# Kernel optimization log

Hardware: AMD Instinct MI355X
Metric: run time of the kernel (lower is better)

The kernel has to match this reference:

```python
import math
import jax, jax.numpy as jnp
import numpy as np

HID, NHEADS, MEM, LIM = 1024, 16, 512, 2048
HEAD = HID // NHEADS  # 64


def _skew(X, pad_value):
    # shift row m right by m steps: [B, M, L] -> [B, M, M+L]
    B, M, L = X.shape
    X = jnp.pad(X, ((0, 0), (0, 0), (0, M + 1)), constant_values=pad_value)
    X = X.reshape(B, -1)[:, :-M]
    return X.reshape(B, M, M + L)


def _unskew(X):
    # reverse of _skew: [B, M, M+L] -> [B, M, L]
    B, M, LM = X.shape
    L = LM - M
    X = jnp.pad(X.reshape(B, -1), ((0, 0), (0, M)))
    return X.reshape(B, M, LM + 1)[:, :, :L]


def _heads(x):
    # [B, S, K*D] -> [B*K, S, D]
    B, S, _ = x.shape
    return x.reshape(B, S, NHEADS, HEAD).transpose(0, 2, 1, 3).reshape(B * NHEADS, S, HEAD)


def setup_inputs() -> dict:
    key = jax.random.key(0)
    ks = jax.random.split(key, 8)
    B = 8
    s = 1.0 / math.sqrt(HID)
    return {
        "query": jax.random.normal(ks[0], (B, MEM, HID), jnp.float32),
        "key": jax.random.normal(ks[1], (B, MEM + LIM, HID), jnp.float32),
        "value": jax.random.normal(ks[2], (B, MEM + LIM, HID), jnp.float32),
        "key_pe": jax.random.normal(ks[3], (1, HEAD, LIM), jnp.float32),
        "Wq": jax.random.normal(ks[4], (HID, HID), jnp.float32) * s,
        "Wk": jax.random.normal(ks[5], (HID, HID), jnp.float32) * s,
        "Wv": jax.random.normal(ks[6], (HID, HID), jnp.float32) * s,
        "Wo": jax.random.normal(ks[7], (HID, HID), jnp.float32) * s,
    }


def reference(query, key, value, key_pe, Wq, Wk, Wv, Wo):
    B = query.shape[0]
    q = _heads(query @ Wq.T)   # [B*K, M, D]
    k = _heads(key @ Wk.T)     # [B*K, M+L, D]
    v = _heads(value @ Wv.T)   # [B*K, M+L, D]
    # content term via skew/unskew trick
    attn_cont = _unskew(jnp.einsum('bmd,bnd->bmn', q, k))  # [B*K, M, L]
    # relative-position term
    attn_pos = jnp.einsum('bmd,dl->bml', q, key_pe[0])     # [B*K, M, L]
    attn = jax.nn.softmax((attn_cont + attn_pos) / math.sqrt(HEAD), axis=-1)
    out = jnp.matmul(_skew(attn, 0.0), v)                  # [B*K, M, D]
    out = out.reshape(B, NHEADS, MEM, HEAD).transpose(0, 2, 1, 3).reshape(B, MEM, HID)
    return out @ Wo.T
```

## Files before the change

### kernel.cpp

```cpp
#include <hip/hip_runtime.h>
#include <hip/hip_bf16.h>
#include <stdint.h>


typedef __attribute__((ext_vector_type(8))) __bf16 bfrag;
typedef __attribute__((ext_vector_type(4))) float f4;

#define DEVFN static __device__ __forceinline__

DEVFN void glds16(const void* g, void* l) {
  __builtin_amdgcn_global_load_lds((const __attribute__((address_space(1))) void*)g,
                                   (__attribute__((address_space(3))) void*)l, 16, 0, 0);
}

DEVFN bfrag cvt8(const float* p) {
  f4 a = *(const f4*)p;
  f4 b = *(const f4*)(p + 4);
  bfrag v;
  v[0] = (__bf16)a.x; v[1] = (__bf16)a.y; v[2] = (__bf16)a.z; v[3] = (__bf16)a.w;
  v[4] = (__bf16)b.x; v[5] = (__bf16)b.y; v[6] = (__bf16)b.z; v[7] = (__bf16)b.w;
  return v;
}

__global__ __launch_bounds__(256) void conv4(const float* __restrict__ a0, const float* __restrict__ a1,
                                             const float* __restrict__ a2, const float* __restrict__ a3,
                                             __bf16* __restrict__ d0, __bf16* __restrict__ d1,
                                             __bf16* __restrict__ d2, __bf16* __restrict__ d3) {
  int bx = blockIdx.x;
  int sel = bx >> 9;
  const float* s = sel == 0 ? a0 : sel == 1 ? a1 : sel == 2 ? a2 : a3;
  __bf16* d = sel == 0 ? d0 : sel == 1 ? d1 : sel == 2 ? d2 : d3;
  int i = ((bx & 511) * 256 + (int)threadIdx.x) * 8;
  *(bfrag*)(d + i) = cvt8(s + i);
}

__global__ __launch_bounds__(256) void convin(const float* __restrict__ q, const float* __restrict__ k,
                                              const float* __restrict__ v,
                                              __bf16* __restrict__ qd, __bf16* __restrict__ kd,
                                              __bf16* __restrict__ vd) {
  int bx = blockIdx.x;
  const float* s; __bf16* d; int lb;
  if (bx < 2048)       { s = q; d = qd; lb = bx; }
  else if (bx < 12288) { s = k; d = kd; lb = bx - 2048; }
  else                 { s = v; d = vd; lb = bx - 12288; }
  int i = (lb * 256 + (int)threadIdx.x) * 8;
  *(bfrag*)(d + i) = cvt8(s + i);
}

__global__ __launch_bounds__(256) void pek(const float* __restrict__ pe,
                                           __bf16* __restrict__ peT) {
  int i = blockIdx.x * 256 + threadIdx.x;
  if (i < 64 * 2048) {
    int d = i >> 11, l = i & 2047;
    peT[(size_t)(l + 64) * 64 + d] = (__bf16)pe[i];
  } else {
    int zi = i - 64 * 2048;
    int row = zi >> 6, dd = zi & 63;
    int r = row < 64 ? row : (2112 + row - 64);
    peT[(size_t)r * 64 + dd] = (__bf16)0.f;
  }
}

DEVFN void stageA_row(const float* ap, __bf16* lds, int arow, int ahalf) {
  const f4* p = (const f4*)ap;
#pragma unroll
  for (int q = 0; q < 4; ++q) {
    f4 a = p[2 * q], b = p[2 * q + 1];
    bfrag v;
    v[0] = (__bf16)a.x; v[1] = (__bf16)a.y; v[2] = (__bf16)a.z; v[3] = (__bf16)a.w;
    v[4] = (__bf16)b.x; v[5] = (__bf16)b.y; v[6] = (__bf16)b.z; v[7] = (__bf16)b.w;
    int ch = (4 * ahalf + q) ^ (arow & 7);
    *(bfrag*)&lds[arow * 64 + ch * 8] = v;
  }
}

template <int AMODE, typename AT>
__global__ __launch_bounds__(256) void projk(const AT* __restrict__ Aq, const AT* __restrict__ Ak,
                                             const AT* __restrict__ Av,
                                             const __bf16* __restrict__ Wqb, const __bf16* __restrict__ Wkb,
                                             const __bf16* __restrict__ Wvb,
                                             __bf16* __restrict__ qws, __bf16* __restrict__ kws,
                                             __bf16* __restrict__ vtws) {
  __shared__ alignas(16) __bf16 Alds[128 * 64];
  __shared__ alignas(16) __bf16 Blds[128 * 64];
  int bx = blockIdx.x;
  const AT* A; const __bf16* B; __bf16* C; int nb, lb, rpb, trans;
  if (bx < 256)       { A = Aq; B = Wqb; C = qws;  lb = bx;        nb = 256;  rpb = 4;  trans = 0; }
  else if (bx < 1536) { A = Ak; B = Wkb; C = kws;  lb = bx - 256;  nb = 1280; rpb = 20; trans = 0; }
  else                { A = Av; B = Wvb; C = vtws; lb = bx - 1536; nb = 1280; rpb = 20; trans = 1; }

  const int tid = threadIdx.x;
  const int lane = tid & 63, wv = tid >> 6;
  const int wr = wv >> 1, wc = wv & 1;
  const int g = lane >> 4, cl = lane & 15;

  int v = (lb & 7) * (nb >> 3) + (lb >> 3);
  const int trow = v >> 3;
  const int r0 = trow * 128, c0 = (v & 7) * 128;

  f4 acc[4][4] = {};

  for (int k0 = 0; k0 < 1024; k0 += 64) {
    __syncthreads();
#pragma unroll
    for (int i = 0; i < 4; ++i) {
      int slot = tid + 256 * i;
      int row = slot >> 3, ch = slot & 7;
      glds16(B + (size_t)(c0 + row) * 1024 + k0 + ((ch ^ (row & 7)) << 3),
             &Blds[slot << 3]);
      if constexpr (AMODE == 1)
        glds16(A + (size_t)(r0 + row) * 1024 + k0 + ((ch ^ (row & 7)) << 3),
               &Alds[slot << 3]);
    }
    if constexpr (AMODE == 0)
      stageA_row(A + (size_t)(r0 + (tid >> 1)) * 1024 + k0 + (tid & 1) * 32,
                 Alds, tid >> 1, tid & 1);
    __syncthreads();
#pragma unroll
    for (int kc = 0; kc < 2; ++kc) {
      bfrag af[4], bfv[4];
#pragma unroll
      for (int i = 0; i < 4; ++i) {
        int rA = 64 * wr + 16 * i + cl;
        af[i] = *(const bfrag*)&Alds[rA * 64 + (((g + 4 * kc) ^ (rA & 7)) << 3)];
        int rB = 64 * wc + 16 * i + cl;
        bfv[i] = *(const bfrag*)&Blds[rB * 64 + (((g + 4 * kc) ^ (rB & 7)) << 3)];
      }
#pragma unroll
      for (int am = 0; am < 4; ++am)
#pragma unroll
        for (int bn = 0; bn < 4; ++bn)
          acc[am][bn] =
              __builtin_amdgcn_mfma_f32_16x16x32_bf16(af[am], bfv[bn], acc[am][bn], 0, 0, 0);
    }
  }

  int Sseq = rpb << 7;
  int b = trow / rpb;
  int sbase = r0 - b * Sseq;
#pragma unroll
  for (int am = 0; am < 4; ++am)
#pragma unroll
    for (int bn = 0; bn < 4; ++bn) {
      int jg = c0 + 64 * wc + 16 * bn + cl;
      int h = jg >> 6, d = jg & 63;
#pragma unroll
      for (int r = 0; r < 4; ++r) {
        int s = sbase + 64 * wr + 16 * am + 4 * g + r;
        size_t dst = trans ? ((size_t)(b * 16 + h) * 64 + d) * 2560 + s
                           : ((size_t)(b * 16 + h) * Sseq + s) * 64 + d;
        C[dst] = (__bf16)acc[am][bn][r];
      }
    }
}

__global__ __launch_bounds__(256) void gemm_out(const __bf16* __restrict__ A,
                                                const __bf16* __restrict__ B,
                                                float* __restrict__ C) {
  __shared__ alignas(16) __bf16 Alds[128 * 64];
  __shared__ alignas(16) __bf16 Blds[128 * 64];
  const int tid = threadIdx.x;
  const int lane = tid & 63, wv = tid >> 6;
  const int wr = wv >> 1, wc = wv & 1;
  const int g = lane >> 4, cl = lane & 15;

  int bx = blockIdx.x;
  int v = (bx & 7) * 32 + (bx >> 3);
  const int r0 = (v >> 3) * 128, c0 = (v & 7) * 128;

  f4 acc[4][4] = {};
  for (int k0 = 0; k0 < 1024; k0 += 64) {
    __syncthreads();
#pragma unroll
    for (int i = 0; i < 4; ++i) {
      int slot = tid + 256 * i;
      int row = slot >> 3, ch = slot & 7;
      glds16(B + (size_t)(c0 + row) * 1024 + k0 + ((ch ^ (row & 7)) << 3),
             &Blds[slot << 3]);
      glds16(A + (size_t)(r0 + row) * 1024 + k0 + ((ch ^ (row & 7)) << 3),
             &Alds[slot << 3]);
    }
    __syncthreads();
#pragma unroll
    for (int kc = 0; kc < 2; ++kc) {
      bfrag af[4], bfv[4];
#pragma unroll
      for (int i = 0; i < 4; ++i) {
        int rA = 64 * wr + 16 * i + cl;
        af[i] = *(const bfrag*)&Alds[rA * 64 + (((g + 4 * kc) ^ (rA & 7)) << 3)];
        int rB = 64 * wc + 16 * i + cl;
        bfv[i] = *(const bfrag*)&Blds[rB * 64 + (((g + 4 * kc) ^ (rB & 7)) << 3)];
      }
#pragma unroll
      for (int am = 0; am < 4; ++am)
#pragma unroll
        for (int bn = 0; bn < 4; ++bn)
          acc[am][bn] =
              __builtin_amdgcn_mfma_f32_16x16x32_bf16(af[am], bfv[bn], acc[am][bn], 0, 0, 0);
    }
  }
#pragma unroll
  for (int am = 0; am < 4; ++am)
#pragma unroll
    for (int bn = 0; bn < 4; ++bn)
#pragma unroll
      for (int r = 0; r < 4; ++r) {
        int rg = r0 + 64 * wr + 16 * am + 4 * g + r;
        int jg = c0 + 64 * wc + 16 * bn + cl;
        C[(size_t)rg * 1024 + jg] = acc[am][bn][r];
      }
}

#define SCL 0.18033688011112042f
#define FMX 20.0f

__global__ __launch_bounds__(256) void attnk(const __bf16* __restrict__ qws,
                                             const __bf16* __restrict__ kws,
                                             const __bf16* __restrict__ vtws,
                                             const __bf16* __restrict__ pews,
                                             __bf16* __restrict__ obuf) {
  __shared__ alignas(16) __bf16 Ks[64 * 64];
  __shared__ alignas(16) __bf16 QVs[64 * 64];
  __shared__ alignas(16) __bf16 PPs[64 * 64];
  __shared__ alignas(16) __bf16 Pbs[64 * 128];

  int bx = blockIdx.x;
  int vv = (bx & 7) * 128 + (bx >> 3);
  int bh = vv >> 3, mt = vv & 7;
  int m0 = mt * 64;
  const __bf16* qb = qws + (size_t)bh * 512 * 64;
  const __bf16* kb = kws + (size_t)bh * 2560 * 64;
  const __bf16* vb = vtws + (size_t)bh * 64 * 2560;

  const int tid = threadIdx.x;
  const int lane = tid & 63, w = tid >> 6;
  const int g = lane >> 4, cl = lane & 15;

#pragma unroll
  for (int i = 0; i < 2; ++i) {
    int slot = tid + 256 * i;
    int row = slot >> 3, ch = slot & 7;
    glds16(qb + (size_t)(m0 + row) * 64 + ((ch ^ (row & 7)) << 3), &QVs[slot << 3]);
  }
  __syncthreads();
  bfrag qf_all[4][2];
#pragma unroll
  for (int rb = 0; rb < 4; ++rb) {
    int rq = 16 * rb + cl;
#pragma unroll
    for (int kc = 0; kc < 2; ++kc)
      qf_all[rb][kc] = *(const bfrag*)&QVs[rq * 64 + (((g + 4 * kc) ^ (rq & 7)) << 3)];
  }

  f4 o[4] = {};
  float lsum[4] = {};

  for (int t = 0; t < 33; ++t) {
    int n0 = m0 + 64 * t;
    __syncthreads();
#pragma unroll
    for (int i = 0; i < 2; ++i) {
      int slot = tid + 256 * i;
      int row = slot >> 3, ch = slot & 7;
      glds16(kb + (size_t)(n0 + row) * 64 + ((ch ^ (row & 7)) << 3), &Ks[slot << 3]);
      glds16(vb + (size_t)row * 2560 + n0 + ((ch ^ (row & 7)) << 3), &QVs[slot << 3]);
      glds16(pews + (size_t)(64 * (t + 1) + row) * 64 + ((ch ^ (row & 7)) << 3),
             &PPs[slot << 3]);
    }
    __syncthreads();

    f4 sc[4] = {};
    __builtin_amdgcn_s_setprio(1);
#pragma unroll
    for (int kc = 0; kc < 2; ++kc)
#pragma unroll
      for (int cb = 0; cb < 4; ++cb) {
        int rk = 16 * cb + cl;
        bfrag kf = *(const bfrag*)&Ks[rk * 64 + (((g + 4 * kc) ^ (rk & 7)) << 3)];
        sc[cb] = __builtin_amdgcn_mfma_f32_16x16x32_bf16(qf_all[w][kc], kf, sc[cb], 0, 0, 0);
      }
    f4 pbacc[4] = {};
#pragma unroll
    for (int kc = 0; kc < 2; ++kc) {
      int rp = 16 * w + cl;
      bfrag pf = *(const bfrag*)&PPs[rp * 64 + (((g + 4 * kc) ^ (rp & 7)) << 3)];
#pragma unroll
      for (int rb = 0; rb < 4; ++rb)
        pbacc[rb] = __builtin_amdgcn_mfma_f32_16x16x32_bf16(qf_all[rb][kc], pf, pbacc[rb], 0, 0, 0);
    }
    __builtin_amdgcn_s_setprio(0);
    {
      int half = (t & 1) << 6;
      int c2 = 16 * w + cl;
#pragma unroll
      for (int rb = 0; rb < 4; ++rb)
#pragma unroll
        for (int r = 0; r < 4; ++r)
          Pbs[(16 * rb + 4 * g + r) * 128 + half + c2] = (__bf16)pbacc[rb][r];
    }
    __syncthreads();

    bool edge = (t == 0) || (t == 32);
#pragma unroll
    for (int r = 0; r < 4; ++r) {
      int jm = 16 * w + 4 * g + r;
#pragma unroll
      for (int cb = 0; cb < 4; ++cb) {
        int jn = 16 * cb + cl;
        int l = 64 * t + jn - jm;
        float pv = (float)Pbs[jm * 128 + (l & 127)];
        float ex = fmaf(sc[cb][r] + pv, SCL, -FMX);
        if (edge) ex = ((unsigned)l < 2048u) ? ex : -1e30f;
        float p = __builtin_amdgcn_exp2f(ex);
        lsum[r] += p;
        PPs[jm * 64 + (((jn >> 3) ^ (jm & 7)) << 3) + (jn & 7)] = (__bf16)p;
      }
    }

    __builtin_amdgcn_s_setprio(1);
#pragma unroll
    for (int kc = 0; kc < 2; ++kc) {
      int rp2 = 16 * w + cl;
      bfrag pa = *(const bfrag*)&PPs[rp2 * 64 + (((g + 4 * kc) ^ (rp2 & 7)) << 3)];
#pragma unroll
      for (int cb = 0; cb < 4; ++cb) {
        int rv = 16 * cb + cl;
        bfrag vf = *(const bfrag*)&QVs[rv * 64 + (((g + 4 * kc) ^ (rv & 7)) << 3)];
        o[cb] = __builtin_amdgcn_mfma_f32_16x16x32_bf16(pa, vf, o[cb], 0, 0, 0);
      }
    }
    __builtin_amdgcn_s_setprio(0);
  }

#pragma unroll
  for (int r = 0; r < 4; ++r)
#pragma unroll
    for (int off = 1; off < 16; off <<= 1) lsum[r] += __shfl_xor(lsum[r], off);

  int b = bh >> 4, h = bh & 15;
#pragma unroll
  for (int cb = 0; cb < 4; ++cb)
#pragma unroll
    for (int r = 0; r < 4; ++r) {
      int m = m0 + 16 * w + 4 * g + r;
      int d = 16 * cb + cl;
      obuf[((size_t)(b * 512 + m)) * 1024 + h * 64 + d] = (__bf16)(o[cb][r] / lsum[r]);
    }
}

extern "C" void kernel_launch(void* const* d_in, const int* in_sizes, int n_in,
                              void* d_out, int out_size, void* d_ws, size_t ws_size,
                              hipStream_t stream) {
  const float* query = (const float*)d_in[0];
  const float* key   = (const float*)d_in[1];
  const float* value = (const float*)d_in[2];
  const float* keype = (const float*)d_in[3];
  const float* Wq    = (const float*)d_in[4];
  const float* Wk    = (const float*)d_in[5];
  const float* Wv    = (const float*)d_in[6];
  const float* Wo    = (const float*)d_in[7];
  float* out = (float*)d_out;
  (void)in_sizes; (void)n_in; (void)out_size;

  char* ws = (char*)d_ws;
  size_t off = 0;
  auto alloc = [&](size_t bytes) {
    void* p = ws + off;
    off += (bytes + 255) & ~(size_t)255;
    return p;
  };
  __bf16* Wqb  = (__bf16*)alloc((size_t)1024 * 1024 * 2);
  __bf16* Wkb  = (__bf16*)alloc((size_t)1024 * 1024 * 2);
  __bf16* Wvb  = (__bf16*)alloc((size_t)1024 * 1024 * 2);
  __bf16* Wob  = (__bf16*)alloc((size_t)1024 * 1024 * 2);
  __bf16* peT  = (__bf16*)alloc((size_t)2176 * 64 * 2);
  __bf16* qws  = (__bf16*)alloc((size_t)128 * 512 * 64 * 2);
  __bf16* kws  = (__bf16*)alloc((size_t)128 * 2560 * 64 * 2);
  __bf16* vtws = (__bf16*)alloc((size_t)128 * 2560 * 64 * 2);

  const size_t NEED = (size_t)194 * 1024 * 1024;
  bool big = ws_size >= NEED;

  conv4<<<2048, 256, 0, stream>>>(Wq, Wk, Wv, Wo, Wqb, Wkb, Wvb, Wob);
  pek<<<544, 256, 0, stream>>>(keype, peT);

  __bf16* obuf;
  if (big) {
    __bf16* qbf = (__bf16*)alloc((size_t)8 * 512 * 1024 * 2);
    __bf16* kbf = (__bf16*)alloc((size_t)8 * 2560 * 1024 * 2);
    __bf16* vbf = (__bf16*)alloc((size_t)8 * 2560 * 1024 * 2);
    obuf = qbf;
    convin<<<22528, 256, 0, stream>>>(query, key, value, qbf, kbf, vbf);
    projk<1, __bf16><<<2816, 256, 0, stream>>>(qbf, kbf, vbf, Wqb, Wkb, Wvb,
                                               qws, kws, vtws);
  } else {
    obuf = (__bf16*)alloc((size_t)4096 * 1024 * 2);
    projk<0, float><<<2816, 256, 0, stream>>>(query, key, value, Wqb, Wkb, Wvb,
                                              qws, kws, vtws);
  }

  attnk<<<1024, 256, 0, stream>>>(qws, kws, vtws, peT, obuf);
  gemm_out<<<256, 256, 0, stream>>>(obuf, Wob, out);
}
```

Measured before the change: 395.0 us.

## Replace bf16 projection GEMM with 256x256-tile double-buffered 8-wave kernel

```diff
diff --git a/kernel.cpp b/kernel.cpp
--- a/kernel.cpp
+++ b/kernel.cpp
@@ -61,6 +61,156 @@
   }
 }
 
+DEVFN bfrag rdfrag(const __bf16* L, int row, int kc, int g) {
+  return *(const bfrag*)&L[row * 64 + (((g + 4 * kc) ^ (row & 7)) << 3)];
+}
+
+__global__ __launch_bounds__(512, 2) void projk8(const __bf16* __restrict__ qbf,
+                                                 const __bf16* __restrict__ kbf,
+                                                 const __bf16* __restrict__ vbf,
+                                                 const __bf16* __restrict__ Wqb,
+                                                 const __bf16* __restrict__ Wkb,
+                                                 const __bf16* __restrict__ Wvb,
+                                                 __bf16* __restrict__ qws,
+                                                 __bf16* __restrict__ kws,
+                                                 __bf16* __restrict__ vtws) {
+  __shared__ alignas(16) __bf16 AL[2][256 * 64];
+  __shared__ alignas(16) __bf16 BL[2][256 * 64];
+
+  int bx = blockIdx.x;
+  int v = (bx & 7) * 88 + (bx >> 3);
+  int rt = v >> 2, ct = v & 3;
+
+  const __bf16* A; const __bf16* W; __bf16* C; int lrt, S, trans;
+  if (rt < 16)      { A = qbf; W = Wqb; C = qws;  lrt = rt;      S = 512;  trans = 0; }
+  else if (rt < 96) { A = kbf; W = Wkb; C = kws;  lrt = rt - 16; S = 2560; trans = 0; }
+  else              { A = vbf; W = Wvb; C = vtws; lrt = rt - 96; S = 2560; trans = 1; }
+  const int r0 = lrt * 256, c0 = ct * 256;
+  const size_t aoff = (size_t)r0 * 1024, boff = (size_t)c0 * 1024;
+
+  const int tid = threadIdx.x;
+  const int lane = tid & 63, wv = tid >> 6;
+  const int wr = wv >> 2, wc = wv & 3;
+  const int g = lane >> 4, cl = lane & 15;
+
+  auto stage_half = [&](int s, int k0, int h) {
+#pragma unroll
+    for (int j = 0; j < 2; ++j) {
+      int slot = h * 1024 + j * 512 + tid;
+      int row = slot >> 3, ch = slot & 7;
+      size_t gof = (size_t)row * 1024 + k0 + ((ch ^ (row & 7)) << 3);
+      glds16(A + aoff + gof, &AL[s][slot << 3]);
+      glds16(W + boff + gof, &BL[s][slot << 3]);
+    }
+  };
+
+  f4 acc[8][4] = {};
+
+  stage_half(0, 0, 0);
+  stage_half(0, 0, 1);
+  asm volatile("s_waitcnt vmcnt(0)" ::: "memory");
+  __builtin_amdgcn_s_barrier();
+
+  for (int kt = 0; kt < 16; ++kt) {
+    const int s = kt & 1;
+    const __bf16* As = AL[s];
+    const __bf16* Bs = BL[s];
+    const int k0n = (kt + 1) * 64;
+    bfrag af[8], b01[4], b23[4];
+
+#pragma unroll
+    for (int mf = 0; mf < 4; ++mf)
+#pragma unroll
+      for (int kc = 0; kc < 2; ++kc)
+        af[mf * 2 + kc] = rdfrag(As, wr * 128 + mf * 16 + cl, kc, g);
+#pragma unroll
+    for (int nf = 0; nf < 2; ++nf)
+#pragma unroll
+      for (int kc = 0; kc < 2; ++kc)
+        b01[nf * 2 + kc] = rdfrag(Bs, wc * 64 + nf * 16 + cl, kc, g);
+    if (kt < 15) stage_half(s ^ 1, k0n, 0);
+    __builtin_amdgcn_s_barrier();
+    __builtin_amdgcn_s_setprio(1);
+#pragma unroll
+    for (int mf = 0; mf < 4; ++mf)
+#pragma unroll
+      for (int nf = 0; nf < 2; ++nf)
+#pragma unroll
+        for (int kc = 0; kc < 2; ++kc)
+          acc[mf][nf] = __builtin_amdgcn_mfma_f32_16x16x32_bf16(
+              af[mf * 2 + kc], b01[nf * 2 + kc], acc[mf][nf], 0, 0, 0);
+    __builtin_amdgcn_s_setprio(0);
+    __builtin_amdgcn_s_barrier();
+
+#pragma unroll
+    for (int nf = 0; nf < 2; ++nf)
+#pragma unroll
+      for (int kc = 0; kc < 2; ++kc)
+        b23[nf * 2 + kc] = rdfrag(Bs, wc * 64 + (2 + nf) * 16 + cl, kc, g);
+    if (kt < 15) stage_half(s ^ 1, k0n, 1);
+    __builtin_amdgcn_s_barrier();
+    __builtin_amdgcn_s_setprio(1);
+#pragma unroll
+    for (int mf = 0; mf < 4; ++mf)
+#pragma unroll
+      for (int nf = 0; nf < 2; ++nf)
+#pragma unroll
+        for (int kc = 0; kc < 2; ++kc)
+          acc[mf][2 + nf] = __builtin_amdgcn_mfma_f32_16x16x32_bf16(
+              af[mf * 2 + kc], b23[nf * 2 + kc], acc[mf][2 + nf], 0, 0, 0);
+    __builtin_amdgcn_s_setprio(0);
+    __builtin_amdgcn_s_barrier();
+
+#pragma unroll
+    for (int mf = 0; mf < 4; ++mf)
+#pragma unroll
+      for (int kc = 0; kc < 2; ++kc)
+        af[mf * 2 + kc] = rdfrag(As, wr * 128 + (4 + mf) * 16 + cl, kc, g);
+    __builtin_amdgcn_s_barrier();
+    __builtin_amdgcn_s_setprio(1);
+#pragma unroll
+    for (int mf = 0; mf < 4; ++mf)
+#pragma unroll
+      for (int nf = 0; nf < 2; ++nf)
+#pragma unroll
+        for (int kc = 0; kc < 2; ++kc)
+          acc[4 + mf][nf] = __builtin_amdgcn_mfma_f32_16x16x32_bf16(
+              af[mf * 2 + kc], b01[nf * 2 + kc], acc[4 + mf][nf], 0, 0, 0);
+    __builtin_amdgcn_s_setprio(0);
+    __builtin_amdgcn_s_barrier();
+
+    __builtin_amdgcn_s_setprio(1);
+#pragma unroll
+    for (int mf = 0; mf < 4; ++mf)
+#pragma unroll
+      for (int nf = 0; nf < 2; ++nf)
+#pragma unroll
+        for (int kc = 0; kc < 2; ++kc)
+          acc[4 + mf][2 + nf] = __builtin_amdgcn_mfma_f32_16x16x32_bf16(
+              af[mf * 2 + kc], b23[nf * 2 + kc], acc[4 + mf][2 + nf], 0, 0, 0);
+    __builtin_amdgcn_s_setprio(0);
+    if (kt < 15) asm volatile("s_waitcnt vmcnt(0)" ::: "memory");
+    __builtin_amdgcn_s_barrier();
+  }
+
+  int b = r0 / S;
+  int sbase = r0 - b * S;
+#pragma unroll
+  for (int mf = 0; mf < 8; ++mf)
+#pragma unroll
+    for (int nf = 0; nf < 4; ++nf) {
+      int jg = c0 + wc * 64 + nf * 16 + cl;
+      int h = jg >> 6, d = jg & 63;
+#pragma unroll
+      for (int r = 0; r < 4; ++r) {
+        int srow = sbase + wr * 128 + mf * 16 + 4 * g + r;
+        size_t dst = trans ? ((size_t)(b * 16 + h) * 64 + d) * 2560 + srow
+                           : ((size_t)(b * 16 + h) * S + srow) * 64 + d;
+        C[dst] = (__bf16)acc[mf][nf][r];
+      }
+    }
+}
+
 DEVFN void stageA_row(const float* ap, __bf16* lds, int arow, int ahalf) {
   const f4* p = (const f4*)ap;
 #pragma unroll
@@ -74,17 +224,16 @@
   }
 }
 
-template <int AMODE, typename AT>
-__global__ __launch_bounds__(256) void projk(const AT* __restrict__ Aq, const AT* __restrict__ Ak,
-                                             const AT* __restrict__ Av,
-                                             const __bf16* __restrict__ Wqb, const __bf16* __restrict__ Wkb,
-                                             const __bf16* __restrict__ Wvb,
-                                             __bf16* __restrict__ qws, __bf16* __restrict__ kws,
-                                             __bf16* __restrict__ vtws) {
+__global__ __launch_bounds__(256) void projk_f32(const float* __restrict__ Aq, const float* __restrict__ Ak,
+                                                 const float* __restrict__ Av,
+                                                 const __bf16* __restrict__ Wqb, const __bf16* __restrict__ Wkb,
+                                                 const __bf16* __restrict__ Wvb,
+                                                 __bf16* __restrict__ qws, __bf16* __restrict__ kws,
+                                                 __bf16* __restrict__ vtws) {
   __shared__ alignas(16) __bf16 Alds[128 * 64];
   __shared__ alignas(16) __bf16 Blds[128 * 64];
   int bx = blockIdx.x;
-  const AT* A; const __bf16* B; __bf16* C; int nb, lb, rpb, trans;
+  const float* A; const __bf16* B; __bf16* C; int nb, lb, rpb, trans;
   if (bx < 256)       { A = Aq; B = Wqb; C = qws;  lb = bx;        nb = 256;  rpb = 4;  trans = 0; }
   else if (bx < 1536) { A = Ak; B = Wkb; C = kws;  lb = bx - 256;  nb = 1280; rpb = 20; trans = 0; }
   else                { A = Av; B = Wvb; C = vtws; lb = bx - 1536; nb = 1280; rpb = 20; trans = 1; }
@@ -108,13 +257,9 @@
       int row = slot >> 3, ch = slot & 7;
       glds16(B + (size_t)(c0 + row) * 1024 + k0 + ((ch ^ (row & 7)) << 3),
              &Blds[slot << 3]);
-      if constexpr (AMODE == 1)
-        glds16(A + (size_t)(r0 + row) * 1024 + k0 + ((ch ^ (row & 7)) << 3),
-               &Alds[slot << 3]);
-    }
-    if constexpr (AMODE == 0)
-      stageA_row(A + (size_t)(r0 + (tid >> 1)) * 1024 + k0 + (tid & 1) * 32,
-                 Alds, tid >> 1, tid & 1);
+    }
+    stageA_row(A + (size_t)(r0 + (tid >> 1)) * 1024 + k0 + (tid & 1) * 32,
+               Alds, tid >> 1, tid & 1);
     __syncthreads();
 #pragma unroll
     for (int kc = 0; kc < 2; ++kc) {
@@ -391,12 +536,11 @@
     __bf16* vbf = (__bf16*)alloc((size_t)8 * 2560 * 1024 * 2);
     obuf = qbf;
     convin<<<22528, 256, 0, stream>>>(query, key, value, qbf, kbf, vbf);
-    projk<1, __bf16><<<2816, 256, 0, stream>>>(qbf, kbf, vbf, Wqb, Wkb, Wvb,
-                                               qws, kws, vtws);
+    projk8<<<704, 512, 0, stream>>>(qbf, kbf, vbf, Wqb, Wkb, Wvb, qws, kws, vtws);
   } else {
     obuf = (__bf16*)alloc((size_t)4096 * 1024 * 2);
-    projk<0, float><<<2816, 256, 0, stream>>>(query, key, value, Wqb, Wkb, Wvb,
-                                              qws, kws, vtws);
+    projk_f32<<<2816, 256, 0, stream>>>(query, key, value, Wqb, Wkb, Wvb,
+                                        qws, kws, vtws);
   }
 
   attnk<<<1024, 256, 0, stream>>>(qws, kws, vtws, peT, obuf);
```

Result: slower. 407.6 us (+3.2%).

## Double-buffer A tile in projection and output GEMMs with prefetch and MFMA priority

Applied to the files above, without the earlier changes.

```diff
diff --git a/kernel.cpp b/kernel.cpp
--- a/kernel.cpp
+++ b/kernel.cpp
@@ -61,6 +61,111 @@
   }
 }
 
+DEVFN bfrag rdfrag(const __bf16* L, int row, int kc, int g) {
+  return *(const bfrag*)&L[row * 64 + (((g + 4 * kc) ^ (row & 7)) << 3)];
+}
+
+DEVFN void core16(const __bf16* __restrict__ A, const __bf16* __restrict__ B,
+                  __bf16* AL, __bf16* BL, f4 (&acc)[4][4],
+                  int tid, int wr, int wc, int g, int cl) {
+  auto stageA = [&](int s, int k0) {
+#pragma unroll
+    for (int j = 0; j < 4; ++j) {
+      int slot = j * 256 + tid;
+      int row = slot >> 3, ch = slot & 7;
+      glds16(A + (size_t)row * 1024 + k0 + ((ch ^ (row & 7)) << 3),
+             &AL[s * 8192 + (slot << 3)]);
+    }
+  };
+  auto stageB = [&](int k0) {
+#pragma unroll
+    for (int j = 0; j < 4; ++j) {
+      int slot = j * 256 + tid;
+      int row = slot >> 3, ch = slot & 7;
+      glds16(B + (size_t)row * 1024 + k0 + ((ch ^ (row & 7)) << 3),
+             &BL[slot << 3]);
+    }
+  };
+
+  stageA(0, 0);
+  for (int kt = 0; kt < 16; ++kt) {
+    const int s = kt & 1;
+    stageB(kt * 64);
+    if (kt < 15) {
+      stageA(s ^ 1, (kt + 1) * 64);
+      asm volatile("s_waitcnt vmcnt(4)" ::: "memory");
+    } else {
+      asm volatile("s_waitcnt vmcnt(0)" ::: "memory");
+    }
+    __builtin_amdgcn_s_barrier();
+    const __bf16* As = &AL[s * 8192];
+#pragma unroll
+    for (int kc = 0; kc < 2; ++kc) {
+      bfrag af[4], bf[4];
+#pragma unroll
+      for (int i = 0; i < 4; ++i) {
+        af[i] = rdfrag(As, 64 * wr + 16 * i + cl, kc, g);
+        bf[i] = rdfrag(BL, 64 * wc + 16 * i + cl, kc, g);
+      }
+      __builtin_amdgcn_s_setprio(1);
+#pragma unroll
+      for (int am = 0; am < 4; ++am)
+#pragma unroll
+        for (int bn = 0; bn < 4; ++bn)
+          acc[am][bn] =
+              __builtin_amdgcn_mfma_f32_16x16x32_bf16(af[am], bf[bn], acc[am][bn], 0, 0, 0);
+      __builtin_amdgcn_s_setprio(0);
+    }
+    __builtin_amdgcn_s_barrier();
+  }
+}
+
+__global__ __launch_bounds__(256) void projk_c(const __bf16* __restrict__ Aq, const __bf16* __restrict__ Ak,
+                                               const __bf16* __restrict__ Av,
+                                               const __bf16* __restrict__ Wqb, const __bf16* __restrict__ Wkb,
+                                               const __bf16* __restrict__ Wvb,
+                                               __bf16* __restrict__ qws, __bf16* __restrict__ kws,
+                                               __bf16* __restrict__ vtws) {
+  __shared__ alignas(16) __bf16 AL[2 * 128 * 64];
+  __shared__ alignas(16) __bf16 BL[128 * 64];
+  int bx = blockIdx.x;
+  const __bf16* A; const __bf16* B; __bf16* C; int nb, lb, rpb, trans;
+  if (bx < 256)       { A = Aq; B = Wqb; C = qws;  lb = bx;        nb = 256;  rpb = 4;  trans = 0; }
+  else if (bx < 1536) { A = Ak; B = Wkb; C = kws;  lb = bx - 256;  nb = 1280; rpb = 20; trans = 0; }
+  else                { A = Av; B = Wvb; C = vtws; lb = bx - 1536; nb = 1280; rpb = 20; trans = 1; }
+
+  const int tid = threadIdx.x;
+  const int lane = tid & 63, wv = tid >> 6;
+  const int wr = wv >> 1, wc = wv & 1;
+  const int g = lane >> 4, cl = lane & 15;
+
+  int v = (lb & 7) * (nb >> 3) + (lb >> 3);
+  const int trow = v >> 3;
+  const int r0 = trow * 128, c0 = (v & 7) * 128;
+
+  f4 acc[4][4] = {};
+  core16(A + (size_t)r0 * 1024, B + (size_t)c0 * 1024, AL, BL, acc,
+         tid, wr, wc, g, cl);
+
+  int Sseq = rpb << 7;
+  int b = trow / rpb;
+  int sbase = r0 - b * Sseq;
+#pragma unroll
+  for (int am = 0; am < 4; ++am)
+#pragma unroll
+    for (int bn = 0; bn < 4; ++bn) {
+      int jg = c0 + 64 * wc + 16 * bn + cl;
+      int h = jg >> 6, d = jg & 63;
+#pragma unroll
+      for (int r = 0; r < 4; ++r) {
+        int s = sbase + 64 * wr + 16 * am + 4 * g + r;
+        size_t dst = trans ? ((size_t)(b * 16 + h) * 64 + d) * 2560 + s
+                           : ((size_t)(b * 16 + h) * Sseq + s) * 64 + d;
+        C[dst] = (__bf16)acc[am][bn][r];
+      }
+    }
+}
+
 DEVFN void stageA_row(const float* ap, __bf16* lds, int arow, int ahalf) {
   const f4* p = (const f4*)ap;
 #pragma unroll
@@ -74,17 +179,16 @@
   }
 }
 
-template <int AMODE, typename AT>
-__global__ __launch_bounds__(256) void projk(const AT* __restrict__ Aq, const AT* __restrict__ Ak,
-                                             const AT* __restrict__ Av,
-                                             const __bf16* __restrict__ Wqb, const __bf16* __restrict__ Wkb,
-                                             const __bf16* __restrict__ Wvb,
-                                             __bf16* __restrict__ qws, __bf16* __restrict__ kws,
-                                             __bf16* __restrict__ vtws) {
+__global__ __launch_bounds__(256) void projk_f32(const float* __restrict__ Aq, const float* __restrict__ Ak,
+                                                 const float* __restrict__ Av,
+                                                 const __bf16* __restrict__ Wqb, const __bf16* __restrict__ Wkb,
+                                                 const __bf16* __restrict__ Wvb,
+                                                 __bf16* __restrict__ qws, __bf16* __restrict__ kws,
+                                                 __bf16* __restrict__ vtws) {
   __shared__ alignas(16) __bf16 Alds[128 * 64];
   __shared__ alignas(16) __bf16 Blds[128 * 64];
   int bx = blockIdx.x;
-  const AT* A; const __bf16* B; __bf16* C; int nb, lb, rpb, trans;
+  const float* A; const __bf16* B; __bf16* C; int nb, lb, rpb, trans;
   if (bx < 256)       { A = Aq; B = Wqb; C = qws;  lb = bx;        nb = 256;  rpb = 4;  trans = 0; }
   else if (bx < 1536) { A = Ak; B = Wkb; C = kws;  lb = bx - 256;  nb = 1280; rpb = 20; trans = 0; }
   else                { A = Av; B = Wvb; C = vtws; lb = bx - 1536; nb = 1280; rpb = 20; trans = 1; }
@@ -108,13 +212,9 @@
       int row = slot >> 3, ch = slot & 7;
       glds16(B + (size_t)(c0 + row) * 1024 + k0 + ((ch ^ (row & 7)) << 3),
              &Blds[slot << 3]);
-      if constexpr (AMODE == 1)
-        glds16(A + (size_t)(r0 + row) * 1024 + k0 + ((ch ^ (row & 7)) << 3),
-               &Alds[slot << 3]);
-    }
-    if constexpr (AMODE == 0)
-      stageA_row(A + (size_t)(r0 + (tid >> 1)) * 1024 + k0 + (tid & 1) * 32,
-                 Alds, tid >> 1, tid & 1);
+    }
+    stageA_row(A + (size_t)(r0 + (tid >> 1)) * 1024 + k0 + (tid & 1) * 32,
+               Alds, tid >> 1, tid & 1);
     __syncthreads();
 #pragma unroll
     for (int kc = 0; kc < 2; ++kc) {
@@ -157,8 +257,8 @@
 __global__ __launch_bounds__(256) void gemm_out(const __bf16* __restrict__ A,
                                                 const __bf16* __restrict__ B,
                                                 float* __restrict__ C) {
-  __shared__ alignas(16) __bf16 Alds[128 * 64];
-  __shared__ alignas(16) __bf16 Blds[128 * 64];
+  __shared__ alignas(16) __bf16 AL[2 * 128 * 64];
+  __shared__ alignas(16) __bf16 BL[128 * 64];
   const int tid = threadIdx.x;
   const int lane = tid & 63, wv = tid >> 6;
   const int wr = wv >> 1, wc = wv & 1;
@@ -169,36 +269,9 @@
   const int r0 = (v >> 3) * 128, c0 = (v & 7) * 128;
 
   f4 acc[4][4] = {};
-  for (int k0 = 0; k0 < 1024; k0 += 64) {
-    __syncthreads();
-#pragma unroll
-    for (int i = 0; i < 4; ++i) {
-      int slot = tid + 256 * i;
-      int row = slot >> 3, ch = slot & 7;
-      glds16(B + (size_t)(c0 + row) * 1024 + k0 + ((ch ^ (row & 7)) << 3),
-             &Blds[slot << 3]);
-      glds16(A + (size_t)(r0 + row) * 1024 + k0 + ((ch ^ (row & 7)) << 3),
-             &Alds[slot << 3]);
-    }
-    __syncthreads();
-#pragma unroll
-    for (int kc = 0; kc < 2; ++kc) {
-      bfrag af[4], bfv[4];
-#pragma unroll
-      for (int i = 0; i < 4; ++i) {
-        int rA = 64 * wr + 16 * i + cl;
-        af[i] = *(const bfrag*)&Alds[rA * 64 + (((g + 4 * kc) ^ (rA & 7)) << 3)];
-        int rB = 64 * wc + 16 * i + cl;
-        bfv[i] = *(const bfrag*)&Blds[rB * 64 + (((g + 4 * kc) ^ (rB & 7)) << 3)];
-      }
-#pragma unroll
-      for (int am = 0; am < 4; ++am)
-#pragma unroll
-        for (int bn = 0; bn < 4; ++bn)
-          acc[am][bn] =
-              __builtin_amdgcn_mfma_f32_16x16x32_bf16(af[am], bfv[bn], acc[am][bn], 0, 0, 0);
-    }
-  }
+  core16(A + (size_t)r0 * 1024, B + (size_t)c0 * 1024, AL, BL, acc,
+         tid, wr, wc, g, cl);
+
 #pragma unroll
   for (int am = 0; am < 4; ++am)
 #pragma unroll
@@ -391,12 +464,11 @@
     __bf16* vbf = (__bf16*)alloc((size_t)8 * 2560 * 1024 * 2);
     obuf = qbf;
     convin<<<22528, 256, 0, stream>>>(query, key, value, qbf, kbf, vbf);
-    projk<1, __bf16><<<2816, 256, 0, stream>>>(qbf, kbf, vbf, Wqb, Wkb, Wvb,
-                                               qws, kws, vtws);
+    projk_c<<<2816, 256, 0, stream>>>(qbf, kbf, vbf, Wqb, Wkb, Wvb, qws, kws, vtws);
   } else {
     obuf = (__bf16*)alloc((size_t)4096 * 1024 * 2);
-    projk<0, float><<<2816, 256, 0, stream>>>(query, key, value, Wqb, Wkb, Wvb,
-                                              qws, kws, vtws);
+    projk_f32<<<2816, 256, 0, stream>>>(query, key, value, Wqb, Wkb, Wvb,
+                                        qws, kws, vtws);
   }
 
   attnk<<<1024, 256, 0, stream>>>(qws, kws, vtws, peT, obuf);
```

New measurement: 379.9 us, median of 2. 1.04x faster.
